# Kernel tuning notes

Hardware: AMD Instinct MI355X
Metric: run time of the kernel (lower is better)

## Reference

```python
import jax, jax.numpy as jnp
import numpy as np

B, DIM, H = 262144, 8, 100


def setup_inputs() -> dict:
    key = jax.random.key(0)
    ks = jax.random.split(key, 11)
    zt1 = jax.random.normal(ks[0], (B, DIM), dtype=jnp.float32)
    zt2 = zt1 + 0.05 * jax.random.normal(ks[1], (B, DIM), dtype=jnp.float32)
    dt = 0.01 * jnp.ones((B,), dtype=jnp.float32)
    s_in = 1.0 / np.sqrt(DIM)
    s_h = 1.0 / np.sqrt(H)
    # drift MLP: Linear(dim,100) -> Softplus -> Linear(100,dim)
    W1m = jax.random.normal(ks[2], (H, DIM), dtype=jnp.float32) * s_in
    b1m = jax.random.normal(ks[3], (H,), dtype=jnp.float32) * s_in
    W2m = jax.random.normal(ks[4], (DIM, H), dtype=jnp.float32) * s_h
    b2m = jax.random.normal(ks[5], (DIM,), dtype=jnp.float32) * s_h
    # diffusion net: Linear(dim,100) -> Softplus -> Linear(100,dim)  (diag=True -> n_entries=dim)
    W1d = jax.random.normal(ks[6], (H, DIM), dtype=jnp.float32) * s_in
    b1d = jax.random.normal(ks[7], (H,), dtype=jnp.float32) * s_in
    W2d = jax.random.normal(ks[8], (DIM, H), dtype=jnp.float32) * s_h
    b2d = jax.random.normal(ks[9], (DIM,), dtype=jnp.float32) * s_h
    return dict(zt1=zt1, zt2=zt2, dt=dt, W1m=W1m, b1m=b1m, W2m=W2m, b2m=b2m,
                W1d=W1d, b1d=b1d, W2d=W2d, b2d=b2d)


def reference(zt1, zt2, dt, W1m, b1m, W2m, b2m, W1d, b1d, W2d, b2d):
    dt0 = dt[0]
    # drift: mu = MLP(zt1) * dt
    mu = jnp.dot(jax.nn.softplus(jnp.dot(zt1, W1m.T) + b1m), W2m.T) + b2m  # [B, dim]
    mu = mu * dt0
    # diffusion: D = exp(Dnet(zt1)); diag Cholesky L = diag(D)
    D = jnp.exp(jnp.dot(jax.nn.softplus(jnp.dot(zt1, W1d.T) + b1d), W2d.T) + b2d)  # [B, dim]
    dz = zt2 - zt1
    # diag=True: cov = diag(D^2), precision = diag(1/D^2), logdet(cov) = 2*sum(log D)
    inv_var = 1.0 / (D * D)
    t1 = 2.0 * jnp.sum(jnp.log(D), axis=-1)
    t2 = jnp.sum(dz * dz * inv_var, axis=-1)
    t3 = -2.0 * jnp.sum(dz * mu * inv_var, axis=-1)
    t4 = jnp.sum(mu * mu * inv_var, axis=-1)
    const = jnp.asarray(-DIM / 2.0 * np.log(2.0 * np.pi), dtype=zt1.dtype)
    log_pz2 = const - 0.5 * (t1 + t2 + t3 + t4)
    loss = jnp.sum(-log_pz2)
    return loss, mu, D * jnp.sqrt(dt0)
```

## Files before the change

kernel.cpp:

```cpp
#include <hip/hip_runtime.h>

constexpr int BN = 262144;
constexpr int H_ = 100;
constexpr int HHALF = 50;

__device__ __forceinline__ float softplus_f(float x) {
    return __logf(1.0f + __expf(x));
}

__global__ __launch_bounds__(256) void sde_fused(
    const float* __restrict__ zt1, const float* __restrict__ zt2,
    const float* __restrict__ dtp,
    const float* __restrict__ W1m, const float* __restrict__ b1m,
    const float* __restrict__ W2m, const float* __restrict__ b2m,
    const float* __restrict__ W1d, const float* __restrict__ b1d,
    const float* __restrict__ W2d, const float* __restrict__ b2d,
    float* __restrict__ out)
{
    const int tid  = threadIdx.x;
    const int lane = tid & 63;
    const int wv   = tid >> 6;
    const int pair = wv >> 1;
    const int h    = __builtin_amdgcn_readfirstlane(wv & 1);
    const int row  = blockIdx.x * 128 + pair * 64 + lane;

    const float dt0  = dtp[0];
    const float sqdt = sqrtf(dt0);

    float x[8];
    {
        const float4* p = reinterpret_cast<const float4*>(zt1) + (size_t)row * 2;
        float4 a = p[0], b = p[1];
        x[0]=a.x; x[1]=a.y; x[2]=a.z; x[3]=a.w;
        x[4]=b.x; x[5]=b.y; x[6]=b.z; x[7]=b.w;
    }

    float am[8], ad[8];
    if (h == 0) {
        #pragma unroll
        for (int k = 0; k < 8; ++k) { am[k] = b2m[k]; ad[k] = b2d[k]; }
    } else {
        #pragma unroll
        for (int k = 0; k < 8; ++k) { am[k] = 0.f; ad[k] = 0.f; }
    }

    const int j0 = h * HHALF;
    #pragma unroll 2
    for (int jj = 0; jj < HHALF; ++jj) {
        const int j = j0 + jj;
        float pm = b1m[j], pd = b1d[j];
        #pragma unroll
        for (int k = 0; k < 8; ++k) {
            pm = fmaf(x[k], W1m[j*8 + k], pm);
            pd = fmaf(x[k], W1d[j*8 + k], pd);
        }
        const float hm = softplus_f(pm);
        const float hd = softplus_f(pd);
        #pragma unroll
        for (int k = 0; k < 8; ++k) {
            am[k] = fmaf(hm, W2m[k*H_ + j], am[k]);
            ad[k] = fmaf(hd, W2d[k*H_ + j], ad[k]);
        }
    }

    __shared__ float xch[256 * 9];
    float* mine = &xch[tid * 9];
    if (h == 0) {
        mine[0]=am[4]; mine[1]=am[5]; mine[2]=am[6]; mine[3]=am[7];
        mine[4]=ad[4]; mine[5]=ad[5]; mine[6]=ad[6]; mine[7]=ad[7];
    } else {
        mine[0]=am[0]; mine[1]=am[1]; mine[2]=am[2]; mine[3]=am[3];
        mine[4]=ad[0]; mine[5]=ad[1]; mine[6]=ad[2]; mine[7]=ad[3];
    }
    __syncthreads();
    const float* part = &xch[(tid ^ 64) * 9];

    float* __restrict__ mu_out = out + 1;
    float* __restrict__ sg_out = out + 1 + (size_t)BN * 8;

    float t1 = 0.f, t2 = 0.f, t3 = 0.f, t4 = 0.f;

#define EPI(K0)                                                              \
    {                                                                        \
        const float4 zb = *(reinterpret_cast<const float4*>(zt2) +           \
                            ((size_t)row * 2 + (K0 / 4)));                   \
        const float z2v[4] = {zb.x, zb.y, zb.z, zb.w};                       \
        _Pragma("unroll")                                                    \
        for (int q = 0; q < 4; ++q) {                                        \
            const int k = K0 + q;                                            \
            const float a_m = am[k] + part[q];                               \
            const float a_d = ad[k] + part[4 + q];                           \
            const float mu = a_m * dt0;                                      \
            const float y  = a_d;                        \
            const float Dk = __expf(y);                                      \
            const float iv = __expf(-2.0f * y);                   \
            const float dz = z2v[q] - x[k];                                  \
            t1 += y;                                                         \
            t2 = fmaf(dz * dz, iv, t2);                                      \
            t3 = fmaf(dz * mu, iv, t3);                                      \
            t4 = fmaf(mu * mu, iv, t4);                                      \
            mu_out[(size_t)row * 8 + k] = mu;                                \
            sg_out[(size_t)row * 8 + k] = Dk * sqdt;                         \
        }                                                                    \
    }

    if (h == 0) { EPI(0) } else { EPI(4) }
#undef EPI

    float nll = fmaf(0.5f, (2.0f * t1 + t2 - 2.0f * t3 + t4),
                     3.67575413281869039f);

    #pragma unroll
    for (int off = 32; off > 0; off >>= 1) nll += __shfl_down(nll, off);

    __shared__ float wsum[4];
    if (lane == 0) wsum[wv] = nll;
    __syncthreads();
    if (tid == 0) atomicAdd(out, wsum[0] + wsum[1] + wsum[2] + wsum[3]);
}

extern "C" void kernel_launch(void* const* d_in, const int* in_sizes, int n_in,
                              void* d_out, int out_size, void* d_ws, size_t ws_size,
                              hipStream_t stream) {
    hipMemsetAsync(d_out, 0, sizeof(float), stream);
    sde_fused<<<BN / 128, 256, 0, stream>>>(
        (const float*)d_in[0], (const float*)d_in[1], (const float*)d_in[2],
        (const float*)d_in[3], (const float*)d_in[4],
        (const float*)d_in[5], (const float*)d_in[6],
        (const float*)d_in[7], (const float*)d_in[8],
        (const float*)d_in[9], (const float*)d_in[10],
        (float*)d_out);
}
```

Measured before the change: 145.9 us.

## Stage MLP weights in interleaved LDS layout and prefetch zt2 early

Each block copies both MLPs' weights and biases into shared memory, laid out as one 36-float row per hidden unit. The inner loop then fetches weights with wide ds_read float4 loads instead of the scalar constant loads it used before. The zt2 row is loaded at kernel start so its latency overlaps the MLP compute, and the LDS exchange buffer is reused. This adds a per-block cooperative weight copy, extra barriers and about 14KB of LDS, which may reduce occupancy.

```diff
diff --git a/kernel.cpp b/kernel.cpp
--- a/kernel.cpp
+++ b/kernel.cpp
@@ -3,6 +3,7 @@
 constexpr int BN = 262144;
 constexpr int H_ = 100;
 constexpr int HHALF = 50;
+constexpr int RS = 36;
 
 __device__ __forceinline__ float softplus_f(float x) {
     return __logf(1.0f + __expf(x));
@@ -17,12 +18,30 @@
     const float* __restrict__ W2d, const float* __restrict__ b2d,
     float* __restrict__ out)
 {
+    __shared__ __align__(16) float smem[H_ * RS];
+    __shared__ float wsum[4];
+
     const int tid  = threadIdx.x;
     const int lane = tid & 63;
     const int wv   = tid >> 6;
     const int pair = wv >> 1;
     const int h    = __builtin_amdgcn_readfirstlane(wv & 1);
     const int row  = blockIdx.x * 128 + pair * 64 + lane;
+
+    for (int idx = tid; idx < 800; idx += 256) {
+        const int j = idx >> 3, k = idx & 7;
+        smem[j * RS + 0 + k] = W1m[idx];
+        smem[j * RS + 8 + k] = W1d[idx];
+    }
+    for (int idx = tid; idx < 800; idx += 256) {
+        const int k = idx / 100, j = idx - k * 100;
+        smem[j * RS + 16 + k] = W2m[idx];
+        smem[j * RS + 24 + k] = W2d[idx];
+    }
+    if (tid < H_) {
+        smem[tid * RS + 32] = b1m[tid];
+        smem[tid * RS + 33] = b1d[tid];
+    }
 
     const float dt0  = dtp[0];
     const float sqdt = sqrtf(dt0);
@@ -34,6 +53,11 @@
         x[0]=a.x; x[1]=a.y; x[2]=a.z; x[3]=a.w;
         x[4]=b.x; x[5]=b.y; x[6]=b.z; x[7]=b.w;
     }
+    float4 z2a, z2b;
+    {
+        const float4* p = reinterpret_cast<const float4*>(zt2) + (size_t)row * 2;
+        z2a = p[0]; z2b = p[1];
+    }
 
     float am[8], ad[8];
     if (h == 0) {
@@ -44,27 +68,45 @@
         for (int k = 0; k < 8; ++k) { am[k] = 0.f; ad[k] = 0.f; }
     }
 
-    const int j0 = h * HHALF;
+    __syncthreads();
+
+    const float* __restrict__ base = smem + h * (HHALF * RS);
     #pragma unroll 2
     for (int jj = 0; jj < HHALF; ++jj) {
-        const int j = j0 + jj;
-        float pm = b1m[j], pd = b1d[j];
-        #pragma unroll
-        for (int k = 0; k < 8; ++k) {
-            pm = fmaf(x[k], W1m[j*8 + k], pm);
-            pd = fmaf(x[k], W1d[j*8 + k], pd);
-        }
+        const float* r = base + jj * RS;
+        const float4 w1m0 = *(const float4*)(r + 0);
+        const float4 w1m1 = *(const float4*)(r + 4);
+        const float4 w1d0 = *(const float4*)(r + 8);
+        const float4 w1d1 = *(const float4*)(r + 12);
+        const float2 bb   = *(const float2*)(r + 32);
+        float pm = bb.x, pd = bb.y;
+        pm = fmaf(x[0], w1m0.x, pm); pm = fmaf(x[1], w1m0.y, pm);
+        pm = fmaf(x[2], w1m0.z, pm); pm = fmaf(x[3], w1m0.w, pm);
+        pm = fmaf(x[4], w1m1.x, pm); pm = fmaf(x[5], w1m1.y, pm);
+        pm = fmaf(x[6], w1m1.z, pm); pm = fmaf(x[7], w1m1.w, pm);
+        pd = fmaf(x[0], w1d0.x, pd); pd = fmaf(x[1], w1d0.y, pd);
+        pd = fmaf(x[2], w1d0.z, pd); pd = fmaf(x[3], w1d0.w, pd);
+        pd = fmaf(x[4], w1d1.x, pd); pd = fmaf(x[5], w1d1.y, pd);
+        pd = fmaf(x[6], w1d1.z, pd); pd = fmaf(x[7], w1d1.w, pd);
         const float hm = softplus_f(pm);
         const float hd = softplus_f(pd);
-        #pragma unroll
-        for (int k = 0; k < 8; ++k) {
-            am[k] = fmaf(hm, W2m[k*H_ + j], am[k]);
-            ad[k] = fmaf(hd, W2d[k*H_ + j], ad[k]);
-        }
+        const float4 w2m0 = *(const float4*)(r + 16);
+        const float4 w2m1 = *(const float4*)(r + 20);
+        const float4 w2d0 = *(const float4*)(r + 24);
+        const float4 w2d1 = *(const float4*)(r + 28);
+        am[0] = fmaf(hm, w2m0.x, am[0]); am[1] = fmaf(hm, w2m0.y, am[1]);
+        am[2] = fmaf(hm, w2m0.z, am[2]); am[3] = fmaf(hm, w2m0.w, am[3]);
+        am[4] = fmaf(hm, w2m1.x, am[4]); am[5] = fmaf(hm, w2m1.y, am[5]);
+        am[6] = fmaf(hm, w2m1.z, am[6]); am[7] = fmaf(hm, w2m1.w, am[7]);
+        ad[0] = fmaf(hd, w2d0.x, ad[0]); ad[1] = fmaf(hd, w2d0.y, ad[1]);
+        ad[2] = fmaf(hd, w2d0.z, ad[2]); ad[3] = fmaf(hd, w2d0.w, ad[3]);
+        ad[4] = fmaf(hd, w2d1.x, ad[4]); ad[5] = fmaf(hd, w2d1.y, ad[5]);
+        ad[6] = fmaf(hd, w2d1.z, ad[6]); ad[7] = fmaf(hd, w2d1.w, ad[7]);
     }
 
-    __shared__ float xch[256 * 9];
-    float* mine = &xch[tid * 9];
+    __syncthreads();
+
+    float* mine = smem + tid * 9;
     if (h == 0) {
         mine[0]=am[4]; mine[1]=am[5]; mine[2]=am[6]; mine[3]=am[7];
         mine[4]=ad[4]; mine[5]=ad[5]; mine[6]=ad[6]; mine[7]=ad[7];
@@ -73,18 +115,16 @@
         mine[4]=ad[0]; mine[5]=ad[1]; mine[6]=ad[2]; mine[7]=ad[3];
     }
     __syncthreads();
-    const float* part = &xch[(tid ^ 64) * 9];
+    const float* part = smem + (tid ^ 64) * 9;
 
     float* __restrict__ mu_out = out + 1;
     float* __restrict__ sg_out = out + 1 + (size_t)BN * 8;
 
     float t1 = 0.f, t2 = 0.f, t3 = 0.f, t4 = 0.f;
 
-#define EPI(K0)                                                              \
+#define EPI(K0, ZB)                                                          \
     {                                                                        \
-        const float4 zb = *(reinterpret_cast<const float4*>(zt2) +           \
-                            ((size_t)row * 2 + (K0 / 4)));                   \
-        const float z2v[4] = {zb.x, zb.y, zb.z, zb.w};                       \
+        const float z2v[4] = {ZB.x, ZB.y, ZB.z, ZB.w};                       \
         _Pragma("unroll")                                                    \
         for (int q = 0; q < 4; ++q) {                                        \
             const int k = K0 + q;                                            \
@@ -104,7 +144,7 @@
         }                                                                    \
     }
 
-    if (h == 0) { EPI(0) } else { EPI(4) }
+    if (h == 0) { EPI(0, z2a) } else { EPI(4, z2b) }
 #undef EPI
 
     float nll = fmaf(0.5f, (2.0f * t1 + t2 - 2.0f * t3 + t4),
@@ -113,7 +153,7 @@
     #pragma unroll
     for (int off = 32; off > 0; off >>= 1) nll += __shfl_down(nll, off);
 
-    __shared__ float wsum[4];
+    __syncthreads();
     if (lane == 0) wsum[wv] = nll;
     __syncthreads();
     if (tid == 0) atomicAdd(out, wsum[0] + wsum[1] + wsum[2] + wsum[3]);
```

Result: faster. 137.0 us (-6.1%).

## Pack MLP weights into per-hidden-unit rows and prefetch zt2 early

Applied to the files above, without the earlier changes.

Adds a small pre-pass kernel that repacks W1m, W1d, W2m, W2d and the hidden biases into contiguous 36-float rows per hidden unit in the workspace. The main kernel then reads all per-unit weights with wave-uniform scalar loads from one contiguous row, instead of strided loads from six arrays. The zt2 load is also moved to the start so its latency overlaps the MLP loop. The cost is an extra kernel launch, and the packing is redone on every call.

```diff
diff --git a/kernel.cpp b/kernel.cpp
--- a/kernel.cpp
+++ b/kernel.cpp
@@ -3,20 +3,45 @@
 constexpr int BN = 262144;
 constexpr int H_ = 100;
 constexpr int HHALF = 50;
+constexpr int RS = 36;
 
 __device__ __forceinline__ float softplus_f(float x) {
     return __logf(1.0f + __expf(x));
 }
 
+__global__ __launch_bounds__(256) void pack_w(
+    const float* __restrict__ W1m, const float* __restrict__ b1m,
+    const float* __restrict__ W2m, const float* __restrict__ W1d,
+    const float* __restrict__ b1d, const float* __restrict__ W2d,
+    float* __restrict__ rows)
+{
+    const int gid = blockIdx.x * 256 + threadIdx.x;
+    const int NT  = gridDim.x * 256;
+    for (int idx = gid; idx < 800; idx += NT) {
+        const int j = idx >> 3, k = idx & 7;
+        rows[j * RS + 0 + k] = W1m[idx];
+        rows[j * RS + 8 + k] = W1d[idx];
+    }
+    for (int idx = gid; idx < 800; idx += NT) {
+        const int k = idx / 100, j = idx - k * 100;
+        rows[j * RS + 16 + k] = W2m[idx];
+        rows[j * RS + 24 + k] = W2d[idx];
+    }
+    if (gid < H_) {
+        rows[gid * RS + 32] = b1m[gid];
+        rows[gid * RS + 33] = b1d[gid];
+    }
+}
+
 __global__ __launch_bounds__(256) void sde_fused(
     const float* __restrict__ zt1, const float* __restrict__ zt2,
-    const float* __restrict__ dtp,
-    const float* __restrict__ W1m, const float* __restrict__ b1m,
-    const float* __restrict__ W2m, const float* __restrict__ b2m,
-    const float* __restrict__ W1d, const float* __restrict__ b1d,
-    const float* __restrict__ W2d, const float* __restrict__ b2d,
+    const float* __restrict__ dtp, const float* __restrict__ b2m,
+    const float* __restrict__ b2d, const float* __restrict__ rows,
     float* __restrict__ out)
 {
+    __shared__ float xch[256 * 9];
+    __shared__ float wsum[4];
+
     const int tid  = threadIdx.x;
     const int lane = tid & 63;
     const int wv   = tid >> 6;
@@ -34,6 +59,11 @@
         x[0]=a.x; x[1]=a.y; x[2]=a.z; x[3]=a.w;
         x[4]=b.x; x[5]=b.y; x[6]=b.z; x[7]=b.w;
     }
+    float4 z2a, z2b;
+    {
+        const float4* p = reinterpret_cast<const float4*>(zt2) + (size_t)row * 2;
+        z2a = p[0]; z2b = p[1];
+    }
 
     float am[8], ad[8];
     if (h == 0) {
@@ -44,26 +74,25 @@
         for (int k = 0; k < 8; ++k) { am[k] = 0.f; ad[k] = 0.f; }
     }
 
-    const int j0 = h * HHALF;
+    const float* __restrict__ rbase = rows + h * (HHALF * RS);
     #pragma unroll 2
     for (int jj = 0; jj < HHALF; ++jj) {
-        const int j = j0 + jj;
-        float pm = b1m[j], pd = b1d[j];
+        const float* r = rbase + jj * RS;
+        float pm = r[32], pd = r[33];
         #pragma unroll
         for (int k = 0; k < 8; ++k) {
-            pm = fmaf(x[k], W1m[j*8 + k], pm);
-            pd = fmaf(x[k], W1d[j*8 + k], pd);
+            pm = fmaf(x[k], r[k],     pm);
+            pd = fmaf(x[k], r[8 + k], pd);
         }
         const float hm = softplus_f(pm);
         const float hd = softplus_f(pd);
         #pragma unroll
         for (int k = 0; k < 8; ++k) {
-            am[k] = fmaf(hm, W2m[k*H_ + j], am[k]);
-            ad[k] = fmaf(hd, W2d[k*H_ + j], ad[k]);
+            am[k] = fmaf(hm, r[16 + k], am[k]);
+            ad[k] = fmaf(hd, r[24 + k], ad[k]);
         }
     }
 
-    __shared__ float xch[256 * 9];
     float* mine = &xch[tid * 9];
     if (h == 0) {
         mine[0]=am[4]; mine[1]=am[5]; mine[2]=am[6]; mine[3]=am[7];
@@ -80,11 +109,9 @@
 
     float t1 = 0.f, t2 = 0.f, t3 = 0.f, t4 = 0.f;
 
-#define EPI(K0)                                                              \
+#define EPI(K0, ZB)                                                          \
     {                                                                        \
-        const float4 zb = *(reinterpret_cast<const float4*>(zt2) +           \
-                            ((size_t)row * 2 + (K0 / 4)));                   \
-        const float z2v[4] = {zb.x, zb.y, zb.z, zb.w};                       \
+        const float z2v[4] = {ZB.x, ZB.y, ZB.z, ZB.w};                       \
         _Pragma("unroll")                                                    \
         for (int q = 0; q < 4; ++q) {                                        \
             const int k = K0 + q;                                            \
@@ -104,7 +131,7 @@
         }                                                                    \
     }
 
-    if (h == 0) { EPI(0) } else { EPI(4) }
+    if (h == 0) { EPI(0, z2a) } else { EPI(4, z2b) }
 #undef EPI
 
     float nll = fmaf(0.5f, (2.0f * t1 + t2 - 2.0f * t3 + t4),
@@ -113,7 +140,6 @@
     #pragma unroll
     for (int off = 32; off > 0; off >>= 1) nll += __shfl_down(nll, off);
 
-    __shared__ float wsum[4];
     if (lane == 0) wsum[wv] = nll;
     __syncthreads();
     if (tid == 0) atomicAdd(out, wsum[0] + wsum[1] + wsum[2] + wsum[3]);
@@ -122,12 +148,16 @@
 extern "C" void kernel_launch(void* const* d_in, const int* in_sizes, int n_in,
                               void* d_out, int out_size, void* d_ws, size_t ws_size,
                               hipStream_t stream) {
+    float* rows = (float*)d_ws;
     hipMemsetAsync(d_out, 0, sizeof(float), stream);
+    pack_w<<<4, 256, 0, stream>>>(
+        (const float*)d_in[3], (const float*)d_in[4],
+        (const float*)d_in[5],
+        (const float*)d_in[7], (const float*)d_in[8],
+        (const float*)d_in[9],
+        rows);
     sde_fused<<<BN / 128, 256, 0, stream>>>(
         (const float*)d_in[0], (const float*)d_in[1], (const float*)d_in[2],
-        (const float*)d_in[3], (const float*)d_in[4],
-        (const float*)d_in[5], (const float*)d_in[6],
-        (const float*)d_in[7], (const float*)d_in[8],
-        (const float*)d_in[9], (const float*)d_in[10],
-        (float*)d_out);
+        (const float*)d_in[6], (const float*)d_in[10],
+        rows, (float*)d_out);
 }
```

Result: faster. 138.8 us (-4.9%).
